# Optimization experiments

Measured on AMD Instinct MI355X. Metric: run time of the kernel, lower is better.

Reference implementation:

```python
import jax, jax.numpy as jnp
import numpy as np

INPUT_DIM = 100
HIDDEN = 128
LAYERS = 4
OUT_DIM = 2
B, T = 256, 512


def _xavier(key, shape):
    fan_out, fan_in = shape[0], shape[1]
    limit = float(np.sqrt(6.0 / (fan_in + fan_out)))
    return jax.random.uniform(key, shape, jnp.float32, -limit, limit)


def setup_inputs() -> dict:
    key = jax.random.key(0)
    ks = jax.random.split(key, 1 + 4 * LAYERS + 2)
    inp = {"x": jax.random.normal(ks[0], (B, T, INPUT_DIM), jnp.float32)}
    kidx = 1
    for l in range(LAYERS):
        in_dim = INPUT_DIM if l == 0 else HIDDEN
        inp[f"w_ih_{l}"] = _xavier(ks[kidx], (4 * HIDDEN, in_dim)); kidx += 1
        inp[f"w_hh_{l}"] = _xavier(ks[kidx], (4 * HIDDEN, HIDDEN)); kidx += 1
        # PyTorch default bias init: U(-1/sqrt(H), 1/sqrt(H))
        s = 1.0 / np.sqrt(HIDDEN)
        inp[f"b_ih_{l}"] = jax.random.uniform(ks[kidx], (4 * HIDDEN,), jnp.float32, -s, s); kidx += 1
        inp[f"b_hh_{l}"] = jax.random.uniform(ks[kidx], (4 * HIDDEN,), jnp.float32, -s, s); kidx += 1
    inp["fc_w"] = _xavier(ks[kidx], (OUT_DIM, HIDDEN)); kidx += 1
    s = 1.0 / np.sqrt(HIDDEN)
    inp["fc_b"] = jax.random.uniform(ks[kidx], (OUT_DIM,), jnp.float32, -s, s)
    return inp


def _lstm_layer(x_tbd, w_ih, w_hh, b_ih, b_hh):
    # x_tbd: [T, B, D]. Precompute input projections for all timesteps.
    xg = jnp.einsum('tbd,gd->tbg', x_tbd, w_ih) + b_ih + b_hh  # [T, B, 4H]
    h0 = jnp.zeros((x_tbd.shape[1], HIDDEN), x_tbd.dtype)
    c0 = jnp.zeros_like(h0)

    def step(carry, xg_t):
        h, c = carry
        g = xg_t + h @ w_hh.T  # [B, 4H]; torch gate order i, f, g, o
        i, f, gg, o = jnp.split(g, 4, axis=-1)
        c = jax.nn.sigmoid(f) * c + jax.nn.sigmoid(i) * jnp.tanh(gg)
        h = jax.nn.sigmoid(o) * jnp.tanh(c)
        return (h, c), h

    _, hs = jax.lax.scan(step, (h0, c0), xg)
    return hs  # [T, B, H]


def reference(x,
              w_ih_0, w_hh_0, b_ih_0, b_hh_0,
              w_ih_1, w_hh_1, b_ih_1, b_hh_1,
              w_ih_2, w_hh_2, b_ih_2, b_hh_2,
              w_ih_3, w_hh_3, b_ih_3, b_hh_3,
              fc_w, fc_b):
    params = [(w_ih_0, w_hh_0, b_ih_0, b_hh_0),
              (w_ih_1, w_hh_1, b_ih_1, b_hh_1),
              (w_ih_2, w_hh_2, b_ih_2, b_hh_2),
              (w_ih_3, w_hh_3, b_ih_3, b_hh_3)]
    h = jnp.swapaxes(x, 0, 1)  # [T, B, D]
    for (w_ih, w_hh, b_ih, b_hh) in params:
        h = _lstm_layer(h, w_ih, w_hh, b_ih, b_hh)
    last = h[-1]  # [B, H]; dropout is identity in eval mode
    return last @ fc_w.T + fc_b  # [B, OUT_DIM]
```

## Files before the change

kernel.cpp:

```cpp
#include <hip/hip_runtime.h>
#include <hip/hip_fp16.h>


#define TSTEPS 512
#define BATCH  256
#define HID    128
#define GATES  512
#define TC     32

typedef _Float16 half8 __attribute__((ext_vector_type(8)));
typedef float f32x4 __attribute__((ext_vector_type(4)));

__device__ __forceinline__ float sigmoid_f(float x) {
    return __builtin_amdgcn_rcpf(1.0f + __expf(-x));
}
__device__ __forceinline__ float tanh_f(float x) {
    float e = __expf(2.0f * x);
    return 1.0f - 2.0f * __builtin_amdgcn_rcpf(e + 1.0f);
}

__device__ __forceinline__ f32x4 cvt_xg4(uint2 raw) {
    __half2 a = __builtin_bit_cast(__half2, raw.x);
    __half2 b = __builtin_bit_cast(__half2, raw.y);
    float2 fa = __half22float2(a), fb = __half22float2(b);
    return (f32x4){fa.x, fa.y, fb.x, fb.y};
}

#define DPP8(x) __int_as_float(__builtin_amdgcn_mov_dpp(__float_as_int(x), 0x118, 0xF, 0xF, true))

#define HSLICE ((size_t)TC * BATCH * HID)

__global__ __launch_bounds__(256)
void pack_whh(const float* __restrict__ W0, const float* __restrict__ W1,
              const float* __restrict__ W2, const float* __restrict__ W3,
              unsigned short* __restrict__ out)
{
    int F = blockIdx.x * 256 + threadIdx.x;
    int l = F >> 16;
    int rem = F & 65535;
    const float* W = (l == 0) ? W0 : (l == 1) ? W1 : (l == 2) ? W2 : W3;
    out[F] = __half_as_ushort(__float2half_rn(W[rem]));
}

__global__ __launch_bounds__(256)
void pack_wih(const float* __restrict__ W0, const float* __restrict__ W1,
              const float* __restrict__ W2, const float* __restrict__ W3,
              unsigned short* __restrict__ out)
{
    int F = blockIdx.x * 256 + threadIdx.x;
    int l = F >> 16;
    int rem = F & 65535;
    int row = rem >> 7, kk = rem & 127;
    float v;
    if (l == 0) {
        v = (kk < 100) ? W0[row * 100 + kk] : 0.f;
    } else {
        const float* W = (l == 1) ? W1 : (l == 2) ? W2 : W3;
        v = W[row * 128 + kk];
    }
    out[F] = __half_as_ushort(__float2half_rn(v));
}

__global__ __launch_bounds__(256)
void pack_x16(const float* __restrict__ X, unsigned int* __restrict__ out)
{
    int F = blockIdx.x * 256 + threadIdx.x;
    int kp = F & 63;
    int rowi = F >> 6;
    int t = rowi >> 8, b = rowi & 255;
    const float* src = X + ((size_t)b * TSTEPS + t) * 100 + kp * 2;
    float v0 = (kp * 2     < 100) ? src[0] : 0.f;
    float v1 = (kp * 2 + 1 < 100) ? src[1] : 0.f;
    __half2 hh = __floats2half2_rn(v0, v1);
    out[F] = __builtin_bit_cast(unsigned int, hh);
}

__global__ __attribute__((amdgpu_waves_per_eu(2, 2))) __launch_bounds__(512)
void scan_wave(int k, int lmin,
               const unsigned short* __restrict__ X16,
               const unsigned short* __restrict__ WIH,
               const unsigned short* __restrict__ WHH,
               const float* __restrict__ bih0, const float* __restrict__ bih1,
               const float* __restrict__ bih2, const float* __restrict__ bih3,
               const float* __restrict__ bhh0, const float* __restrict__ bhh1,
               const float* __restrict__ bhh2, const float* __restrict__ bhh3,
               unsigned short* __restrict__ HIOS,
               float* __restrict__ hstb, float* __restrict__ cstb)
{
    __shared__ uint4 hbuf[2][256];
    __shared__ uint2 xglds[4][1024];

    const int slotb = blockIdx.x >> 5;
    const int blk   = blockIdx.x & 31;
    const int l     = lmin + slotb;
    const int c     = k - l;
    const int first = (c == 0);
    const int wrh   = (l < 3);
    const int tid   = threadIdx.x;

    const float* bih = (l == 0) ? bih0 : (l == 1) ? bih1 : (l == 2) ? bih2 : bih3;
    const float* bhh = (l == 0) ? bhh0 : (l == 1) ? bhh1 : (l == 2) ? bhh2 : bhh3;

    if (tid >= 256) {
        const int wx   = (tid >> 6) - 4;
        const int ll   = tid & 63;
        const int s    = ll >> 4;
        const int t15  = ll & 15;
        const int hi   = t15 >> 3;
        const int rowx = t15 & 7;

        const unsigned short* WI = WIH + (size_t)l * 65536;
        half8 wI[4][2][4];
        #pragma unroll
        for (int g = 0; g < 4; ++g)
            #pragma unroll
            for (int us = 0; us < 2; ++us)
                #pragma unroll
                for (int kt = 0; kt < 4; ++kt) {
                    int rowu = g * 128 + 32 * wx + 16 * us + t15;
                    wI[g][us][kt] = *(const half8*)(WI + rowu * 128 + kt * 32 + s * 8);
                }

        f32x4 bias[4][2];
        #pragma unroll
        for (int g = 0; g < 4; ++g)
            #pragma unroll
            for (int us = 0; us < 2; ++us) {
                int j = g * 128 + 32 * wx + 16 * us + 4 * s;
                float4 bi = *(const float4*)&bih[j];
                float4 bh = *(const float4*)&bhh[j];
                bias[g][us] = (f32x4){bi.x + bh.x, bi.y + bh.y, bi.z + bh.z, bi.w + bh.w};
            }

        const unsigned short* xbase = (l == 0)
            ? X16 + (size_t)(c * TC) * (BATCH * HID)
            : HIOS + ((size_t)(l - 1) * 2 + (c & 1)) * HSLICE;
        const unsigned short* xrow = xbase + ((size_t)(blk * 8 + rowx)) * HID + s * 8;

#define XLOAD(DST, ST) {                                                      \
        const unsigned short* p_ = xrow + (size_t)(ST) * (BATCH * HID);       \
        DST[0] = *(const half8*)(p_);                                         \
        DST[1] = *(const half8*)(p_ + 32);                                    \
        DST[2] = *(const half8*)(p_ + 64);                                    \
        DST[3] = *(const half8*)(p_ + 96); }

#define XCOMP(XFR, SLOT) {                                                    \
        f32x4 axx[4][2];                                                      \
        _Pragma("unroll")                                                     \
        for (int g = 0; g < 4; ++g) {                                         \
            axx[g][0] = bias[g][0]; axx[g][1] = bias[g][1];                   \
        }                                                                     \
        _Pragma("unroll")                                                     \
        for (int kt = 0; kt < 4; ++kt) {                                      \
            _Pragma("unroll")                                                 \
            for (int g = 0; g < 4; ++g) {                                     \
                axx[g][0] = __builtin_amdgcn_mfma_f32_16x16x32_f16(wI[g][0][kt], XFR[kt], axx[g][0], 0, 0, 0); \
                axx[g][1] = __builtin_amdgcn_mfma_f32_16x16x32_f16(wI[g][1][kt], XFR[kt], axx[g][1], 0, 0, 0); \
            }                                                                 \
        }                                                                     \
        _Pragma("unroll")                                                     \
        for (int g = 0; g < 4; ++g) {                                         \
            float sh0 = DPP8(axx[g][1][0]);                                   \
            float sh1 = DPP8(axx[g][1][1]);                                   \
            float sh2 = DPP8(axx[g][1][2]);                                   \
            float sh3 = DPP8(axx[g][1][3]);                                   \
            float q0 = hi ? sh0 : axx[g][0][0];                               \
            float q1 = hi ? sh1 : axx[g][0][1];                               \
            float q2 = hi ? sh2 : axx[g][0][2];                               \
            float q3 = hi ? sh3 : axx[g][0][3];                               \
            __half2 pa_ = __floats2half2_rn(q0, q1);                          \
            __half2 pb_ = __floats2half2_rn(q2, q3);                          \
            uint2 v_ = { __builtin_bit_cast(unsigned int, pa_),               \
                         __builtin_bit_cast(unsigned int, pb_) };             \
            xglds[SLOT][g * 256 + wx * 64 + ll] = v_;                         \
        } }

        half8 xfa[4], xfb[4];
        XLOAD(xfa, 0); XLOAD(xfb, 1);
        XCOMP(xfa, 0); XCOMP(xfb, 1);
        XLOAD(xfa, 2); XLOAD(xfb, 3);
        asm volatile("s_waitcnt lgkmcnt(0)");
        __builtin_amdgcn_sched_barrier(0);
        __builtin_amdgcn_s_barrier();
        __builtin_amdgcn_sched_barrier(0);

        for (int st = 0; st < TC; ++st) {
            if ((st & 1) == 0) {
                if (st + 2 < TC) {
                    XCOMP(xfa, ((st + 2) & 3));
                    if (st + 4 < TC) XLOAD(xfa, st + 4);
                }
            } else {
                if (st + 2 < TC) {
                    XCOMP(xfb, ((st + 2) & 3));
                    if (st + 4 < TC) XLOAD(xfb, st + 4);
                }
            }
            __builtin_amdgcn_sched_barrier(0);
            asm volatile("s_waitcnt lgkmcnt(0)");
            __builtin_amdgcn_sched_barrier(0);
            __builtin_amdgcn_s_barrier();
            __builtin_amdgcn_sched_barrier(0);
        }
#undef XCOMP
#undef XLOAD
        return;
    }

    const int w   = tid >> 6;
    const int ll  = tid & 63;
    const int s   = ll >> 4;
    const int t15 = ll & 15;
    const int hi  = t15 >> 3;
    const int row = t15 & 7;
    const int rb  = blk * 8 + row;
    const int u0  = 32 * w + 16 * hi + 4 * s;

    const unsigned short* WH = WHH + (size_t)l * 65536;
    unsigned short* HIO = HIOS + ((size_t)l * 2 + (c & 1)) * HSLICE;
    float* hstate = hstb + (size_t)l * (BATCH * HID);
    float* cstate = cstb + (size_t)l * (BATCH * HID);

    half8 wA[4][2][4];
    #pragma unroll
    for (int g = 0; g < 4; ++g)
        #pragma unroll
        for (int us = 0; us < 2; ++us)
            #pragma unroll
            for (int kt = 0; kt < 4; ++kt) {
                int rowu = g * 128 + 32 * w + 16 * us + t15;
                wA[g][us][kt] = *(const half8*)(WH + rowu * 128 + kt * 32 + s * 8);
            }

    float c0, c1, c2, c3, h0, h1, h2, h3;
    if (first) {
        c0 = c1 = c2 = c3 = 0.f;
        h0 = h1 = h2 = h3 = 0.f;
    } else {
        f32x4 cv = *(const f32x4*)(cstate + rb * HID + u0);
        c0 = cv[0]; c1 = cv[1]; c2 = cv[2]; c3 = cv[3];
        f32x4 hv = *(const f32x4*)(hstate + rb * HID + u0);
        h0 = hv[0]; h1 = hv[1]; h2 = hv[2]; h3 = hv[3];
    }

    const int wchunk = 4 * w + 2 * hi + (s >> 1);
    const int widx = row * 32 + ((wchunk ^ row) << 1) + (s & 1);
    int ridx[4];
    #pragma unroll
    for (int kt = 0; kt < 4; ++kt)
        ridx[kt] = t15 * 16 + ((4 * kt + s) ^ (t15 & 7));

    {
        __half2 pa = __floats2half2_rn(h0, h1);
        __half2 pb = __floats2half2_rn(h2, h3);
        uint2 v = { *(unsigned int*)&pa, *(unsigned int*)&pb };
        ((uint2*)&hbuf[0][0])[widx] = v;
    }
    asm volatile("s_waitcnt lgkmcnt(0)");
    __builtin_amdgcn_sched_barrier(0);
    __builtin_amdgcn_s_barrier();
    __builtin_amdgcn_sched_barrier(0);

#define STEP(ST, RBUF, WBUF)                                                  \
    {                                                                         \
        half8 bf0 = __builtin_bit_cast(half8, hbuf[RBUF][ridx[0]]);           \
        half8 bf1 = __builtin_bit_cast(half8, hbuf[RBUF][ridx[1]]);           \
        half8 bf2 = __builtin_bit_cast(half8, hbuf[RBUF][ridx[2]]);           \
        half8 bf3 = __builtin_bit_cast(half8, hbuf[RBUF][ridx[3]]);           \
        uint2 xr0 = xglds[(ST) & 3][0 * 256 + w * 64 + ll];                   \
        uint2 xr1 = xglds[(ST) & 3][1 * 256 + w * 64 + ll];                   \
        uint2 xr2 = xglds[(ST) & 3][2 * 256 + w * 64 + ll];                   \
        uint2 xr3 = xglds[(ST) & 3][3 * 256 + w * 64 + ll];                   \
        f32x4 acc[4][2];                                                      \
        _Pragma("unroll")                                                     \
        for (int g = 0; g < 4; ++g) {                                         \
            acc[g][0] = (f32x4){0.f, 0.f, 0.f, 0.f};                          \
            acc[g][1] = (f32x4){0.f, 0.f, 0.f, 0.f};                          \
        }                                                                     \
        _Pragma("unroll")                                                     \
        for (int g = 0; g < 4; ++g) {                                         \
            acc[g][0] = __builtin_amdgcn_mfma_f32_16x16x32_f16(wA[g][0][0], bf0, acc[g][0], 0, 0, 0); \
            acc[g][1] = __builtin_amdgcn_mfma_f32_16x16x32_f16(wA[g][1][0], bf0, acc[g][1], 0, 0, 0); \
            acc[g][0] = __builtin_amdgcn_mfma_f32_16x16x32_f16(wA[g][0][1], bf1, acc[g][0], 0, 0, 0); \
            acc[g][1] = __builtin_amdgcn_mfma_f32_16x16x32_f16(wA[g][1][1], bf1, acc[g][1], 0, 0, 0); \
            acc[g][0] = __builtin_amdgcn_mfma_f32_16x16x32_f16(wA[g][0][2], bf2, acc[g][0], 0, 0, 0); \
            acc[g][1] = __builtin_amdgcn_mfma_f32_16x16x32_f16(wA[g][1][2], bf2, acc[g][1], 0, 0, 0); \
            acc[g][0] = __builtin_amdgcn_mfma_f32_16x16x32_f16(wA[g][0][3], bf3, acc[g][0], 0, 0, 0); \
            acc[g][1] = __builtin_amdgcn_mfma_f32_16x16x32_f16(wA[g][1][3], bf3, acc[g][1], 0, 0, 0); \
        }                                                                     \
        f32x4 xf[4];                                                          \
        xf[0] = cvt_xg4(xr0); xf[1] = cvt_xg4(xr1);                           \
        xf[2] = cvt_xg4(xr2); xf[3] = cvt_xg4(xr3);                           \
        float pre[4][4];                                                      \
        _Pragma("unroll")                                                     \
        for (int g = 0; g < 4; ++g) {                                         \
            _Pragma("unroll")                                                 \
            for (int r = 0; r < 4; ++r) {                                     \
                float sh = DPP8(acc[g][1][r]);                                \
                pre[g][r] = (hi ? sh : acc[g][0][r]) + xf[g][r];              \
            }                                                                 \
        }                                                                     \
        c0 = sigmoid_f(pre[1][0]) * c0 + sigmoid_f(pre[0][0]) * tanh_f(pre[2][0]); \
        h0 = sigmoid_f(pre[3][0]) * tanh_f(c0);                               \
        c1 = sigmoid_f(pre[1][1]) * c1 + sigmoid_f(pre[0][1]) * tanh_f(pre[2][1]); \
        h1 = sigmoid_f(pre[3][1]) * tanh_f(c1);                               \
        c2 = sigmoid_f(pre[1][2]) * c2 + sigmoid_f(pre[0][2]) * tanh_f(pre[2][2]); \
        h2 = sigmoid_f(pre[3][2]) * tanh_f(c2);                               \
        c3 = sigmoid_f(pre[1][3]) * c3 + sigmoid_f(pre[0][3]) * tanh_f(pre[2][3]); \
        h3 = sigmoid_f(pre[3][3]) * tanh_f(c3);                               \
        {                                                                     \
            __half2 pa = __floats2half2_rn(h0, h1);                           \
            __half2 pb = __floats2half2_rn(h2, h3);                           \
            uint2 v = { *(unsigned int*)&pa, *(unsigned int*)&pb };           \
            ((uint2*)&hbuf[WBUF][0])[widx] = v;                               \
            if (wrh)                                                          \
                *(uint2*)(HIO + ((size_t)(ST) * BATCH + rb) * HID + u0) = v;  \
        }                                                                     \
        __builtin_amdgcn_sched_barrier(0);                                    \
        asm volatile("s_waitcnt lgkmcnt(0)");                                 \
        __builtin_amdgcn_sched_barrier(0);                                    \
        __builtin_amdgcn_s_barrier();                                         \
        __builtin_amdgcn_sched_barrier(0);                                    \
    }

    for (int st = 0; st < TC; st += 2) {
        STEP(st,     0, 1);
        STEP(st + 1, 1, 0);
    }
#undef STEP

    f32x4 cv = {c0, c1, c2, c3};
    f32x4 hv = {h0, h1, h2, h3};
    *(f32x4*)(cstate + rb * HID + u0) = cv;
    *(f32x4*)(hstate + rb * HID + u0) = hv;
}

__global__ __launch_bounds__(512)
void fc_kernel(const float* __restrict__ hstate, const float* __restrict__ fcw,
               const float* __restrict__ fcb, float* __restrict__ out)
{
    int idx = threadIdx.x;
    int b = idx >> 1, o = idx & 1;
    float acc = fcb[o];
    #pragma unroll
    for (int k = 0; k < HID; ++k)
        acc = fmaf(hstate[b * HID + k], fcw[o * HID + k], acc);
    out[b * 2 + o] = acc;
}

extern "C" void kernel_launch(void* const* d_in, const int* in_sizes, int n_in,
                              void* d_out, int out_size, void* d_ws, size_t ws_size,
                              hipStream_t stream)
{
    const float* x = (const float*)d_in[0];
    const float* w_ih[4]; const float* w_hh[4];
    const float* b_ih[4]; const float* b_hh[4];
    for (int l = 0; l < 4; ++l) {
        w_ih[l] = (const float*)d_in[1 + 4 * l];
        w_hh[l] = (const float*)d_in[2 + 4 * l];
        b_ih[l] = (const float*)d_in[3 + 4 * l];
        b_hh[l] = (const float*)d_in[4 + 4 * l];
    }
    const float* fc_w = (const float*)d_in[17];
    const float* fc_b = (const float*)d_in[18];
    float* out = (float*)d_out;

    char* wsb = (char*)d_ws;
    unsigned short* x16   = (unsigned short*)wsb;
    unsigned short* hio   = (unsigned short*)(wsb + 33554432);
    float*          hst   = (float*)(wsb + 50331648);
    float*          cst   = (float*)(wsb + 50855936);
    unsigned short* wih16 = (unsigned short*)(wsb + 51380224);
    unsigned short* whh16 = (unsigned short*)(wsb + 51904512);

    pack_whh<<<1024, 256, 0, stream>>>(w_hh[0], w_hh[1], w_hh[2], w_hh[3], whh16);
    pack_wih<<<1024, 256, 0, stream>>>(w_ih[0], w_ih[1], w_ih[2], w_ih[3], wih16);
    pack_x16<<<32768, 256, 0, stream>>>(x, (unsigned int*)x16);

    for (int k = 0; k <= 18; ++k) {
        int lmin = (k - 15 > 0) ? k - 15 : 0;
        int lmax = (k < 3) ? k : 3;
        int nv = lmax - lmin + 1;
        scan_wave<<<nv * 32, 512, 0, stream>>>(
            k, lmin, x16, wih16, whh16,
            b_ih[0], b_ih[1], b_ih[2], b_ih[3],
            b_hh[0], b_hh[1], b_hh[2], b_hh[3],
            hio, hst, cst);
    }
    fc_kernel<<<1, 512, 0, stream>>>(hst + 3 * BATCH * HID, fc_w, fc_b, out);
}
```

Before: 986.8 us.

## Fuse input projection into recurrent waves, drop producer warps and LDS staging

Removes the four producer waves that computed input-gate projections into an LDS ring buffer. The recurrent waves now hold both W_hh and W_ih fragments in registers and compute the projection for step t+2 inline, keeping the results in fp32 registers. This removes the LDS round trip and the fp16 rounding of the projection, and halves the block size. In exchange each wave does twice the MFMA work per step on the serial critical path and carries much higher register pressure, now running at one wave per EU.

```diff
diff --git a/kernel.cpp b/kernel.cpp
--- a/kernel.cpp
+++ b/kernel.cpp
@@ -17,13 +17,6 @@
 __device__ __forceinline__ float tanh_f(float x) {
     float e = __expf(2.0f * x);
     return 1.0f - 2.0f * __builtin_amdgcn_rcpf(e + 1.0f);
-}
-
-__device__ __forceinline__ f32x4 cvt_xg4(uint2 raw) {
-    __half2 a = __builtin_bit_cast(__half2, raw.x);
-    __half2 b = __builtin_bit_cast(__half2, raw.y);
-    float2 fa = __half22float2(a), fb = __half22float2(b);
-    return (f32x4){fa.x, fa.y, fb.x, fb.y};
 }
 
 #define DPP8(x) __int_as_float(__builtin_amdgcn_mov_dpp(__float_as_int(x), 0x118, 0xF, 0xF, true))
@@ -75,7 +68,7 @@
     out[F] = __builtin_bit_cast(unsigned int, hh);
 }
 
-__global__ __attribute__((amdgpu_waves_per_eu(2, 2))) __launch_bounds__(512)
+__global__ __attribute__((amdgpu_waves_per_eu(1, 1))) __launch_bounds__(256)
 void scan_wave(int k, int lmin,
                const unsigned short* __restrict__ X16,
                const unsigned short* __restrict__ WIH,
@@ -88,7 +81,6 @@
                float* __restrict__ hstb, float* __restrict__ cstb)
 {
     __shared__ uint4 hbuf[2][256];
-    __shared__ uint2 xglds[4][1024];
 
     const int slotb = blockIdx.x >> 5;
     const int blk   = blockIdx.x & 31;
@@ -100,112 +92,6 @@
 
     const float* bih = (l == 0) ? bih0 : (l == 1) ? bih1 : (l == 2) ? bih2 : bih3;
     const float* bhh = (l == 0) ? bhh0 : (l == 1) ? bhh1 : (l == 2) ? bhh2 : bhh3;
-
-    if (tid >= 256) {
-        const int wx   = (tid >> 6) - 4;
-        const int ll   = tid & 63;
-        const int s    = ll >> 4;
-        const int t15  = ll & 15;
-        const int hi   = t15 >> 3;
-        const int rowx = t15 & 7;
-
-        const unsigned short* WI = WIH + (size_t)l * 65536;
-        half8 wI[4][2][4];
-        #pragma unroll
-        for (int g = 0; g < 4; ++g)
-            #pragma unroll
-            for (int us = 0; us < 2; ++us)
-                #pragma unroll
-                for (int kt = 0; kt < 4; ++kt) {
-                    int rowu = g * 128 + 32 * wx + 16 * us + t15;
-                    wI[g][us][kt] = *(const half8*)(WI + rowu * 128 + kt * 32 + s * 8);
-                }
-
-        f32x4 bias[4][2];
-        #pragma unroll
-        for (int g = 0; g < 4; ++g)
-            #pragma unroll
-            for (int us = 0; us < 2; ++us) {
-                int j = g * 128 + 32 * wx + 16 * us + 4 * s;
-                float4 bi = *(const float4*)&bih[j];
-                float4 bh = *(const float4*)&bhh[j];
-                bias[g][us] = (f32x4){bi.x + bh.x, bi.y + bh.y, bi.z + bh.z, bi.w + bh.w};
-            }
-
-        const unsigned short* xbase = (l == 0)
-            ? X16 + (size_t)(c * TC) * (BATCH * HID)
-            : HIOS + ((size_t)(l - 1) * 2 + (c & 1)) * HSLICE;
-        const unsigned short* xrow = xbase + ((size_t)(blk * 8 + rowx)) * HID + s * 8;
-
-#define XLOAD(DST, ST) {                                                      \
-        const unsigned short* p_ = xrow + (size_t)(ST) * (BATCH * HID);       \
-        DST[0] = *(const half8*)(p_);                                         \
-        DST[1] = *(const half8*)(p_ + 32);                                    \
-        DST[2] = *(const half8*)(p_ + 64);                                    \
-        DST[3] = *(const half8*)(p_ + 96); }
-
-#define XCOMP(XFR, SLOT) {                                                    \
-        f32x4 axx[4][2];                                                      \
-        _Pragma("unroll")                                                     \
-        for (int g = 0; g < 4; ++g) {                                         \
-            axx[g][0] = bias[g][0]; axx[g][1] = bias[g][1];                   \
-        }                                                                     \
-        _Pragma("unroll")                                                     \
-        for (int kt = 0; kt < 4; ++kt) {                                      \
-            _Pragma("unroll")                                                 \
-            for (int g = 0; g < 4; ++g) {                                     \
-                axx[g][0] = __builtin_amdgcn_mfma_f32_16x16x32_f16(wI[g][0][kt], XFR[kt], axx[g][0], 0, 0, 0); \
-                axx[g][1] = __builtin_amdgcn_mfma_f32_16x16x32_f16(wI[g][1][kt], XFR[kt], axx[g][1], 0, 0, 0); \
-            }                                                                 \
-        }                                                                     \
-        _Pragma("unroll")                                                     \
-        for (int g = 0; g < 4; ++g) {                                         \
-            float sh0 = DPP8(axx[g][1][0]);                                   \
-            float sh1 = DPP8(axx[g][1][1]);                                   \
-            float sh2 = DPP8(axx[g][1][2]);                                   \
-            float sh3 = DPP8(axx[g][1][3]);                                   \
-            float q0 = hi ? sh0 : axx[g][0][0];                               \
-            float q1 = hi ? sh1 : axx[g][0][1];                               \
-            float q2 = hi ? sh2 : axx[g][0][2];                               \
-            float q3 = hi ? sh3 : axx[g][0][3];                               \
-            __half2 pa_ = __floats2half2_rn(q0, q1);                          \
-            __half2 pb_ = __floats2half2_rn(q2, q3);                          \
-            uint2 v_ = { __builtin_bit_cast(unsigned int, pa_),               \
-                         __builtin_bit_cast(unsigned int, pb_) };             \
-            xglds[SLOT][g * 256 + wx * 64 + ll] = v_;                         \
-        } }
-
-        half8 xfa[4], xfb[4];
-        XLOAD(xfa, 0); XLOAD(xfb, 1);
-        XCOMP(xfa, 0); XCOMP(xfb, 1);
-        XLOAD(xfa, 2); XLOAD(xfb, 3);
-        asm volatile("s_waitcnt lgkmcnt(0)");
-        __builtin_amdgcn_sched_barrier(0);
-        __builtin_amdgcn_s_barrier();
-        __builtin_amdgcn_sched_barrier(0);
-
-        for (int st = 0; st < TC; ++st) {
-            if ((st & 1) == 0) {
-                if (st + 2 < TC) {
-                    XCOMP(xfa, ((st + 2) & 3));
-                    if (st + 4 < TC) XLOAD(xfa, st + 4);
-                }
-            } else {
-                if (st + 2 < TC) {
-                    XCOMP(xfb, ((st + 2) & 3));
-                    if (st + 4 < TC) XLOAD(xfb, st + 4);
-                }
-            }
-            __builtin_amdgcn_sched_barrier(0);
-            asm volatile("s_waitcnt lgkmcnt(0)");
-            __builtin_amdgcn_sched_barrier(0);
-            __builtin_amdgcn_s_barrier();
-            __builtin_amdgcn_sched_barrier(0);
-        }
-#undef XCOMP
-#undef XLOAD
-        return;
-    }
 
     const int w   = tid >> 6;
     const int ll  = tid & 63;
@@ -217,6 +103,7 @@
     const int u0  = 32 * w + 16 * hi + 4 * s;
 
     const unsigned short* WH = WHH + (size_t)l * 65536;
+    const unsigned short* WI = WIH + (size_t)l * 65536;
     unsigned short* HIO = HIOS + ((size_t)l * 2 + (c & 1)) * HSLICE;
     float* hstate = hstb + (size_t)l * (BATCH * HID);
     float* cstate = cstb + (size_t)l * (BATCH * HID);
@@ -231,6 +118,70 @@
                 int rowu = g * 128 + 32 * w + 16 * us + t15;
                 wA[g][us][kt] = *(const half8*)(WH + rowu * 128 + kt * 32 + s * 8);
             }
+    half8 wI[4][2][4];
+    #pragma unroll
+    for (int g = 0; g < 4; ++g)
+        #pragma unroll
+        for (int us = 0; us < 2; ++us)
+            #pragma unroll
+            for (int kt = 0; kt < 4; ++kt) {
+                int rowu = g * 128 + 32 * w + 16 * us + t15;
+                wI[g][us][kt] = *(const half8*)(WI + rowu * 128 + kt * 32 + s * 8);
+            }
+
+    f32x4 bias[4][2];
+    #pragma unroll
+    for (int g = 0; g < 4; ++g)
+        #pragma unroll
+        for (int us = 0; us < 2; ++us) {
+            int j = g * 128 + 32 * w + 16 * us + 4 * s;
+            float4 bi = *(const float4*)&bih[j];
+            float4 bh = *(const float4*)&bhh[j];
+            bias[g][us] = (f32x4){bi.x + bh.x, bi.y + bh.y, bi.z + bh.z, bi.w + bh.w};
+        }
+
+    const unsigned short* xbase = (l == 0)
+        ? X16 + (size_t)(c * TC) * (BATCH * HID)
+        : HIOS + ((size_t)(l - 1) * 2 + (c & 1)) * HSLICE;
+    const unsigned short* xrow = xbase + ((size_t)rb) * HID + s * 8;
+
+#define XLOAD(DST, ST) {                                                      \
+        const unsigned short* p_ = xrow + (size_t)(ST) * (BATCH * HID);       \
+        DST[0] = *(const half8*)(p_);                                         \
+        DST[1] = *(const half8*)(p_ + 32);                                    \
+        DST[2] = *(const half8*)(p_ + 64);                                    \
+        DST[3] = *(const half8*)(p_ + 96); }
+
+#define XPROJ(XFR, XGD) {                                                     \
+        f32x4 ax0_[4], ax1_[4];                                               \
+        _Pragma("unroll")                                                     \
+        for (int g = 0; g < 4; ++g) { ax0_[g] = bias[g][0]; ax1_[g] = bias[g][1]; } \
+        _Pragma("unroll")                                                     \
+        for (int kt = 0; kt < 4; ++kt) {                                      \
+            _Pragma("unroll")                                                 \
+            for (int g = 0; g < 4; ++g) {                                     \
+                ax0_[g] = __builtin_amdgcn_mfma_f32_16x16x32_f16(wI[g][0][kt], XFR[kt], ax0_[g], 0, 0, 0); \
+                ax1_[g] = __builtin_amdgcn_mfma_f32_16x16x32_f16(wI[g][1][kt], XFR[kt], ax1_[g], 0, 0, 0); \
+            }                                                                 \
+        }                                                                     \
+        _Pragma("unroll")                                                     \
+        for (int g = 0; g < 4; ++g) {                                         \
+            float s0_ = DPP8(ax1_[g][0]);                                     \
+            float s1_ = DPP8(ax1_[g][1]);                                     \
+            float s2_ = DPP8(ax1_[g][2]);                                     \
+            float s3_ = DPP8(ax1_[g][3]);                                     \
+            XGD[g][0] = hi ? s0_ : ax0_[g][0];                                \
+            XGD[g][1] = hi ? s1_ : ax0_[g][1];                                \
+            XGD[g][2] = hi ? s2_ : ax0_[g][2];                                \
+            XGD[g][3] = hi ? s3_ : ax0_[g][3];                                \
+        } }
+
+    half8 xfE[4], xfO[4];
+    f32x4 xgE[4], xgO[4];
+    XLOAD(xfE, 0); XLOAD(xfO, 1);
+    XPROJ(xfE, xgE);
+    XPROJ(xfO, xgO);
+    XLOAD(xfE, 2); XLOAD(xfO, 3);
 
     float c0, c1, c2, c3, h0, h1, h2, h3;
     if (first) {
@@ -261,16 +212,12 @@
     __builtin_amdgcn_s_barrier();
     __builtin_amdgcn_sched_barrier(0);
 
-#define STEP(ST, RBUF, WBUF)                                                  \
+#define STEP(ST, RBUF, WBUF, XGCUR, XFRG)                                     \
     {                                                                         \
         half8 bf0 = __builtin_bit_cast(half8, hbuf[RBUF][ridx[0]]);           \
         half8 bf1 = __builtin_bit_cast(half8, hbuf[RBUF][ridx[1]]);           \
         half8 bf2 = __builtin_bit_cast(half8, hbuf[RBUF][ridx[2]]);           \
         half8 bf3 = __builtin_bit_cast(half8, hbuf[RBUF][ridx[3]]);           \
-        uint2 xr0 = xglds[(ST) & 3][0 * 256 + w * 64 + ll];                   \
-        uint2 xr1 = xglds[(ST) & 3][1 * 256 + w * 64 + ll];                   \
-        uint2 xr2 = xglds[(ST) & 3][2 * 256 + w * 64 + ll];                   \
-        uint2 xr3 = xglds[(ST) & 3][3 * 256 + w * 64 + ll];                   \
         f32x4 acc[4][2];                                                      \
         _Pragma("unroll")                                                     \
         for (int g = 0; g < 4; ++g) {                                         \
@@ -288,18 +235,17 @@
             acc[g][0] = __builtin_amdgcn_mfma_f32_16x16x32_f16(wA[g][0][3], bf3, acc[g][0], 0, 0, 0); \
             acc[g][1] = __builtin_amdgcn_mfma_f32_16x16x32_f16(wA[g][1][3], bf3, acc[g][1], 0, 0, 0); \
         }                                                                     \
-        f32x4 xf[4];                                                          \
-        xf[0] = cvt_xg4(xr0); xf[1] = cvt_xg4(xr1);                           \
-        xf[2] = cvt_xg4(xr2); xf[3] = cvt_xg4(xr3);                           \
         float pre[4][4];                                                      \
         _Pragma("unroll")                                                     \
         for (int g = 0; g < 4; ++g) {                                         \
             _Pragma("unroll")                                                 \
             for (int r = 0; r < 4; ++r) {                                     \
                 float sh = DPP8(acc[g][1][r]);                                \
-                pre[g][r] = (hi ? sh : acc[g][0][r]) + xf[g][r];              \
+                pre[g][r] = (hi ? sh : acc[g][0][r]) + XGCUR[g][r];           \
             }                                                                 \
         }                                                                     \
+        if ((ST) + 2 < TC) XPROJ(XFRG, XGCUR);                                \
+        if ((ST) + 4 < TC) XLOAD(XFRG, (ST) + 4);                             \
         c0 = sigmoid_f(pre[1][0]) * c0 + sigmoid_f(pre[0][0]) * tanh_f(pre[2][0]); \
         h0 = sigmoid_f(pre[3][0]) * tanh_f(c0);                               \
         c1 = sigmoid_f(pre[1][1]) * c1 + sigmoid_f(pre[0][1]) * tanh_f(pre[2][1]); \
@@ -324,10 +270,12 @@
     }
 
     for (int st = 0; st < TC; st += 2) {
-        STEP(st,     0, 1);
-        STEP(st + 1, 1, 0);
+        STEP(st,     0, 1, xgE, xfE);
+        STEP(st + 1, 1, 0, xgO, xfO);
     }
 #undef STEP
+#undef XPROJ
+#undef XLOAD
 
     f32x4 cv = {c0, c1, c2, c3};
     f32x4 hv = {h0, h1, h2, h3};
@@ -381,7 +329,7 @@
         int lmin = (k - 15 > 0) ? k - 15 : 0;
         int lmax = (k < 3) ? k : 3;
         int nv = lmax - lmin + 1;
-        scan_wave<<<nv * 32, 512, 0, stream>>>(
+        scan_wave<<<nv * 32, 256, 0, stream>>>(
             k, lmin, x16, wih16, whh16,
             b_ih[0], b_ih[1], b_ih[2], b_ih[3],
             b_hh[0], b_hh[1], b_hh[2], b_hh[3],
```

Result: slower. 1.039 ms (+5.3%).
